# Optimization experiments

Hardware: AMD Instinct MI355X
Metric: run time of the kernel (lower is better)

Reference implementation:

```python
import jax, jax.numpy as jnp
import numpy as np

B, T, C, H, DI = 4, 1024, 1024, 16, 128
TAU = 1.0
LAMBDA_CONF = 0.1
SYS2_THR = 1.0


def _ln(x, w, b):
    mu = x.mean(-1, keepdims=True)
    var = x.var(-1, keepdims=True)
    return (x - mu) * jax.lax.rsqrt(var + 1e-5) * w + b


def setup_inputs() -> dict:
    key = jax.random.key(0)
    ks = jax.random.split(key, 16)
    s = lambda i, shape: jax.random.normal(ks[i], shape, jnp.float32) * 0.02
    return {
        "h": jax.random.normal(ks[0], (B, T, C), jnp.float32),
        "ln_w": jnp.ones((C,), jnp.float32), "ln_b": jnp.zeros((C,), jnp.float32),
        "w_q": s(1, (C, C)), "w_k": s(2, (C, C)), "w_v": s(3, (C, C)),
        "w_o": s(4, (C, C)), "b_o": jnp.zeros((C,), jnp.float32),
        "U": s(5, (C, DI)), "V": s(6, (DI, C)),
        "gamma_w": s(7, (C, 1)), "gamma_b": jnp.zeros((1,), jnp.float32),
        "mass_w": s(8, (C, 1)), "mass_b": jnp.zeros((1,), jnp.float32),
        "eps_w": s(9, (C, 1)), "eps_b": jnp.zeros((1,), jnp.float32),
        "lg_w1": s(10, (C, 4 * C)), "lg_b1": jnp.zeros((4 * C,), jnp.float32),
        "lg_w2": s(11, (4 * C, C)), "lg_b2": jnp.zeros((C,), jnp.float32),
        "mlp_w1": s(12, (C, 4 * C)), "mlp_b1": jnp.zeros((4 * C,), jnp.float32),
        "mlp_w2": s(13, (4 * C, C)), "mlp_b2": jnp.zeros((C,), jnp.float32),
    }


def reference(h, ln_w, ln_b, w_q, w_k, w_v, w_o, b_o, U, V,
              gamma_w, gamma_b, mass_w, mass_b, eps_w, eps_b,
              lg_w1, lg_b1, lg_w2, lg_b2, mlp_w1, mlp_b1, mlp_w2, mlp_b2):
    hd = C // H
    h_norm = _ln(h, ln_w, ln_b)

    # ---- HamiltonianAttention (conservative force field) ----
    q = (h_norm @ w_q).reshape(B, T, H, hd).transpose(0, 2, 1, 3)  # [B,H,T,hd]
    k = (h_norm @ w_k).reshape(B, T, H, hd).transpose(0, 2, 1, 3)
    v = (h_norm @ w_v).reshape(B, T, H, hd).transpose(0, 2, 1, 3)
    scores = jnp.einsum('bhqd,bhkd->bhqk', q, k) / (hd ** 0.5) / TAU
    attn = jax.nn.softmax(scores, axis=-1)
    force = jnp.einsum('bhqk,bhkd->bhqd', attn, v).transpose(0, 2, 1, 3).reshape(B, T, C)
    f_attn = force @ w_o + b_o

    # ---- total force, low-rank projection ----
    f_total = f_attn - LAMBDA_CONF * h_norm
    f_proj = f_total @ U                               # [B,T,DI]

    # ---- FSI (force stability index) ----
    h_mag = jnp.linalg.norm(h_norm, axis=-1)           # [B,T]
    f_mag = jnp.linalg.norm(f_proj, axis=-1)
    fsi = h_mag / (2.0 * f_mag + 1e-6)

    # ---- CognitiveGearbox: per-token mass / timestep ----
    mass = 1.0 + jax.nn.softplus(h @ mass_w + mass_b)  # [B,T,1], mass >= 1
    eps = jax.nn.sigmoid(h @ eps_w + eps_b)            # [B,T,1], eps in (0,1)
    gamma = jax.nn.sigmoid(h_norm @ gamma_w + gamma_b) # [B,T,1] damping gate

    # ---- fused AGI momentum recurrence: m_t = gamma_t*m_{t-1} + (eps_t/mass_t)*f_t ----
    def step(m, inps):
        f_t, g_t, e_t, ms_t = inps                     # [B,DI],[B,1],[B,1],[B,1]
        m = g_t * m + (e_t / ms_t) * f_t
        return m, m

    xs = (f_proj.transpose(1, 0, 2), gamma.transpose(1, 0, 2),
          eps.transpose(1, 0, 2), mass.transpose(1, 0, 2))
    m0 = jnp.zeros((B, DI), h.dtype)
    _, m_seq = jax.lax.scan(step, m0, xs)              # [T,B,DI]
    m_new = m_seq.transpose(1, 0, 2)                   # [B,T,DI]

    # ---- position update + system-2 correction + MLP ----
    velocity = m_new @ V                               # [B,T,C]
    h_new = h + eps * velocity
    hn2 = _ln(h_new, ln_w, ln_b)
    sys2 = jax.nn.gelu(hn2 @ lg_w1 + lg_b1, approximate=False) @ lg_w2 + lg_b2
    gate = jax.nn.sigmoid(mass - SYS2_THR)
    h_final = h_new + gate * sys2
    hn3 = _ln(h_final, ln_w, ln_b)
    h_final = h_final + (jax.nn.gelu(hn3 @ mlp_w1 + mlp_b1, approximate=False) @ mlp_w2 + mlp_b2)
    return (h_final, m_new, fsi)
```

## Files before the change

kernel.cpp:

```cpp
#include <hip/hip_runtime.h>
#include <hip/hip_bf16.h>
#include <math.h>

typedef __attribute__((ext_vector_type(8))) short bf16x8;
typedef __attribute__((ext_vector_type(4))) float f32x4;

#define DEVI __device__ __forceinline__

constexpr int B_ = 4, T_ = 1024, C_ = 1024, H_ = 16, HD_ = 64, DI_ = 128;
constexpr int NTOK = B_ * T_;
constexpr int C4 = 4 * C_;
constexpr int C3 = 3 * C_;
constexpr float LAMBDA_CONF = 0.1f;

DEVI short f2bf(float f) {
  unsigned u = __builtin_bit_cast(unsigned, f);
  u += 0x7fffu + ((u >> 16) & 1u);
  return (short)(u >> 16);
}
DEVI unsigned pk2(float a, float b) {
  return (unsigned)(unsigned short)f2bf(a) | ((unsigned)(unsigned short)f2bf(b) << 16);
}
DEVI float sigm(float x) { return 1.f / (1.f + __expf(-x)); }
DEVI float geluf(float x) { return 0.5f * x * (1.f + erff(x * 0.70710678118654752440f)); }

DEVI void gload16(const void* g, void* l) {
  __builtin_amdgcn_global_load_lds((const __attribute__((address_space(1))) unsigned*)g,
                                   (__attribute__((address_space(3))) unsigned*)l, 16, 0, 0);
}

template <int EPI>
DEVI void epi_store(void* Outp, const float* bias, const float* resid, const float* tokv,
                    int row, int col, int N, float v) {
  size_t idx = (size_t)row * N + col;
  if (EPI == 0) {
    ((float*)Outp)[idx] = v;
  } else if (EPI == 1) {
    ((short*)Outp)[idx] = f2bf(v);
  } else if (EPI == 2) {
    ((short*)Outp)[idx] = f2bf(v + bias[col] - LAMBDA_CONF * resid[idx]);
  } else if (EPI == 3) {
    ((float*)Outp)[idx] = resid[idx] + tokv[row] * v;
  } else if (EPI == 4) {
    float x = v + bias[col];
    ((short*)Outp)[idx] = f2bf(geluf(x));
  } else if (EPI == 5) {
    float x = v + bias[col];
    float g = sigm(tokv[row] - 1.f);
    ((float*)Outp)[idx] = resid[idx] + g * x;
  } else if (EPI == 6) {
    ((float*)Outp)[idx] = resid[idx] + v + bias[col];
  }
}

__global__ __launch_bounds__(256) void transpose_cvt(const float* __restrict__ W,
                                                     short* __restrict__ Wt, int K, int N) {
  __shared__ float s[32][33];
  int n0 = blockIdx.x * 32, k0 = blockIdx.y * 32;
  int tx = threadIdx.x & 31, ty = threadIdx.x >> 5;
#pragma unroll
  for (int i = 0; i < 4; i++)
    s[ty + i * 8][tx] = W[(size_t)(k0 + ty + i * 8) * N + n0 + tx];
  __syncthreads();
#pragma unroll
  for (int i = 0; i < 4; i++)
    Wt[(size_t)(n0 + ty + i * 8) * K + k0 + tx] = f2bf(s[tx][ty + i * 8]);
}

__global__ __launch_bounds__(256) void transpose_v(const short* __restrict__ QKV,
                                                   short* __restrict__ VT) {
  __shared__ short s[32][33];
  int bh = blockIdx.z;
  int b = bh >> 4, h = bh & 15;
  int t0 = blockIdx.x * 32, d0 = blockIdx.y * 32;
  int tx = threadIdx.x & 31, ty = threadIdx.x >> 5;
#pragma unroll
  for (int i = 0; i < 4; i++)
    s[ty + i * 8][tx] =
        QKV[(size_t)(b * T_ + t0 + ty + i * 8) * C3 + 2 * C_ + h * 64 + d0 + tx];
  __syncthreads();
#pragma unroll
  for (int i = 0; i < 4; i++)
    VT[((size_t)bh * 64 + d0 + ty + i * 8) * T_ + t0 + tx] = s[tx][ty + i * 8];
}

DEVI float blk_red(float v, volatile float* sm) {
  int lane = threadIdx.x & 63, wv = threadIdx.x >> 6;
#pragma unroll
  for (int o = 32; o; o >>= 1) v += __shfl_down(v, o);
  __syncthreads();
  if (lane == 0) sm[wv] = v;
  __syncthreads();
  return sm[0] + sm[1] + sm[2] + sm[3];
}

template <int FULL, int WF32>
__global__ __launch_bounds__(256) void ln_kernel(
    const float* __restrict__ X, const float* __restrict__ lnw, const float* __restrict__ lnb,
    float* __restrict__ Out, short* __restrict__ OutBf,
    const float* __restrict__ gw, const float* __restrict__ gb,
    const float* __restrict__ mw, const float* __restrict__ mb,
    const float* __restrict__ ew, const float* __restrict__ eb,
    float* __restrict__ gammaA, float* __restrict__ epsA, float* __restrict__ massA,
    float* __restrict__ coefA, float* __restrict__ hmagA) {
  __shared__ float sm[4];
  int tok = blockIdx.x;
  const float* x = X + (size_t)tok * C_;
  int t4 = threadIdx.x * 4;
  float4 xv = *(const float4*)&x[t4];
  float s = xv.x + xv.y + xv.z + xv.w;
  float ss = xv.x * xv.x + xv.y * xv.y + xv.z * xv.z + xv.w * xv.w;
  s = blk_red(s, sm);
  ss = blk_red(ss, sm);
  float mu = s * (1.f / C_);
  float var = ss * (1.f / C_) - mu * mu;
  float rs = rsqrtf(var + 1e-5f);
  float4 wv = *(const float4*)&lnw[t4];
  float4 bv = *(const float4*)&lnb[t4];
  float4 hn;
  hn.x = (xv.x - mu) * rs * wv.x + bv.x;
  hn.y = (xv.y - mu) * rs * wv.y + bv.y;
  hn.z = (xv.z - mu) * rs * wv.z + bv.z;
  hn.w = (xv.w - mu) * rs * wv.w + bv.w;
  if (WF32) *(float4*)&Out[(size_t)tok * C_ + t4] = hn;
  short4 ob;
  ob.x = f2bf(hn.x); ob.y = f2bf(hn.y); ob.z = f2bf(hn.z); ob.w = f2bf(hn.w);
  *(short4*)&OutBf[(size_t)tok * C_ + t4] = ob;
  if (FULL) {
    float4 gwv = *(const float4*)&gw[t4];
    float4 mwv = *(const float4*)&mw[t4];
    float4 ewv = *(const float4*)&ew[t4];
    float gd = hn.x * gwv.x + hn.y * gwv.y + hn.z * gwv.z + hn.w * gwv.w;
    float md = xv.x * mwv.x + xv.y * mwv.y + xv.z * mwv.z + xv.w * mwv.w;
    float ed = xv.x * ewv.x + xv.y * ewv.y + xv.z * ewv.z + xv.w * ewv.w;
    float h2 = hn.x * hn.x + hn.y * hn.y + hn.z * hn.z + hn.w * hn.w;
    gd = blk_red(gd, sm);
    md = blk_red(md, sm);
    ed = blk_red(ed, sm);
    h2 = blk_red(h2, sm);
    if (threadIdx.x == 0) {
      float g = sigm(gd + gb[0]);
      float xm = md + mb[0];
      float sp = (xm > 20.f) ? xm : log1pf(expf(xm));
      float msv = 1.f + sp;
      float epv = sigm(ed + eb[0]);
      gammaA[tok] = g;
      massA[tok] = msv;
      epsA[tok] = epv;
      coefA[tok] = epv / msv;
      hmagA[tok] = sqrtf(h2);
    }
  }
}

template <int EPI, int NB>
__global__ __launch_bounds__(256, 3) void gemmS(
    const short* __restrict__ A, const short* __restrict__ Bt, void* __restrict__ Outp,
    const float* __restrict__ bias, const float* __restrict__ resid,
    const float* __restrict__ tokv, int M, int N, int K) {
  constexpr int NT = NB / 64;
  constexpr int NFR = NB / 32;
  __shared__ short As[128][32];
  __shared__ short Bs[NB][32];
  int tid = threadIdx.x, lane = tid & 63, w = tid >> 6;
  int wr = w >> 1, wc = w & 1;
  int fr = lane & 15, fg = lane >> 4;
  int xm = (fr >> 1) & 3;
  int nM = M >> 7;
  int cpx = gridDim.x >> 3;
  int bid = (blockIdx.x & 7) * cpx + (blockIdx.x >> 3);
  int bm = (bid % nM) << 7;
  int bn = (bid / nM) * NB;
  f32x4 acc[4][NFR] = {};

  int jsw = (lane & 3) ^ ((lane >> 3) & 3);
  const short* gA = A + (size_t)(bm + w * 32 + (lane >> 2)) * K + (jsw << 3);
  const short* gB;
  if constexpr (NB == 128)
    gB = Bt + (size_t)(bn + w * 32 + (lane >> 2)) * K + (jsw << 3);
  else
    gB = Bt + (size_t)(bn + w * 16 + (lane >> 2)) * K + (jsw << 3);

  for (int kt = 0; kt < K; kt += 32) {
    gload16(gA + kt, &As[w * 32][0]);
    gload16(gA + (size_t)16 * K + kt, &As[w * 32 + 16][0]);
    if constexpr (NB == 128) {
      gload16(gB + kt, &Bs[w * 32][0]);
      gload16(gB + (size_t)16 * K + kt, &Bs[w * 32 + 16][0]);
    } else {
      gload16(gB + kt, &Bs[w * 16][0]);
    }
    __syncthreads();
    bf16x8 af[4], bv[NFR];
#pragma unroll
    for (int i = 0; i < 4; i++)
      af[i] = *(const bf16x8*)&As[wr * 64 + i * 16 + fr][(fg ^ xm) << 3];
#pragma unroll
    for (int j = 0; j < NFR; j++)
      bv[j] = *(const bf16x8*)&Bs[wc * (NB / 2) + j * 16 + fr][(fg ^ xm) << 3];
#pragma unroll
    for (int mi = 0; mi < 4; mi++)
#pragma unroll
      for (int ni = 0; ni < NFR; ni++)
        acc[mi][ni] = __builtin_amdgcn_mfma_f32_16x16x32_bf16(af[mi], bv[ni], acc[mi][ni], 0, 0, 0);
    __syncthreads();
  }

#pragma unroll
  for (int mi = 0; mi < 4; mi++) {
    int row0 = bm + wr * 64 + mi * 16 + fg * 4;
#pragma unroll
    for (int ni = 0; ni < NFR; ni++) {
      int col = bn + wc * (NB / 2) + ni * 16 + fr;
#pragma unroll
      for (int r = 0; r < 4; r++)
        epi_store<EPI>(Outp, bias, resid, tokv, row0 + r, col, N, acc[mi][ni][r]);
    }
  }
}

template <int EPI, int MT, int NT>
__global__ __launch_bounds__(512) void gemmP(
    const short* __restrict__ A, const short* __restrict__ Bt, void* __restrict__ Outp,
    const float* __restrict__ bias, const float* __restrict__ resid,
    const float* __restrict__ tokv, int M, int N, int K) {
  constexpr int BM = 4 * MT * 16;
  constexpr int BN = 2 * NT * 16;
  constexpr int CA = BM / 64;
  constexpr int CB = BN / 64;
  constexpr int LPT = CA + CB;
  __shared__ short As[3][BM][64];
  __shared__ short Bs[3][BN][64];
  int tid = threadIdx.x, lane = tid & 63, w = tid >> 6;
  int wr = w >> 1, wc = w & 1;
  int fr = lane & 15, fg = lane >> 4;
  int nMt = M / BM;
  int cpx = gridDim.x >> 3;
  int gbid = (blockIdx.x & 7) * cpx + (blockIdx.x >> 3);
  int chunk = gbid >> 5;
  int wi = gbid & 31;
  int nCM = nMt >> 2;
  int bm = ((chunk % nCM) * 4 + (wi & 3)) * BM;
  int bn = ((chunk / nCM) * 8 + (wi >> 2)) * BN;
  f32x4 acc[MT][NT] = {};

  int jsw = (lane & 7) ^ ((lane >> 3) & 7);
  const short* gA = A + (size_t)(bm + w * 8 + (lane >> 3)) * K + (jsw << 3);
  const short* gB = Bt + (size_t)(bn + w * 8 + (lane >> 3)) * K + (jsw << 3);

  auto stage = [&](int buf, int kt) {
#pragma unroll
    for (int c = 0; c < CA; c++)
      gload16(gA + (size_t)(c * 64) * K + kt, &As[buf][c * 64 + w * 8][0]);
#pragma unroll
    for (int c = 0; c < CB; c++)
      gload16(gB + (size_t)(c * 64) * K + kt, &Bs[buf][c * 64 + w * 8][0]);
  };

  int nt = K >> 6;
  stage(0, 0);
  if (nt > 1) stage(1, 64);
  for (int t = 0; t < nt; t++) {
    if (t + 1 < nt) {
      if constexpr (LPT == 6) asm volatile("s_waitcnt vmcnt(6)" ::: "memory");
      else asm volatile("s_waitcnt vmcnt(4)" ::: "memory");
    } else {
      asm volatile("s_waitcnt vmcnt(0)" ::: "memory");
    }
    __builtin_amdgcn_s_barrier();
    __builtin_amdgcn_sched_barrier(0);
    int nb = t + 2;
    if (nb < nt) stage(nb % 3, nb << 6);
    int cb = t % 3;
    short(*Ac)[64] = As[cb];
    short(*Bc)[64] = Bs[cb];
    bf16x8 af[MT], bv[NT / 2];
#pragma unroll
    for (int kh = 0; kh < 2; kh++) {
#pragma unroll
      for (int i = 0; i < MT; i++) {
        int row = wr * (MT * 16) + i * 16 + fr;
        af[i] = *(const bf16x8*)&Ac[row][((((kh << 2) | fg)) ^ (fr & 7)) << 3];
      }
#pragma unroll
      for (int nh = 0; nh < 2; nh++) {
#pragma unroll
        for (int j = 0; j < NT / 2; j++) {
          int row = wc * (NT * 16) + nh * (NT / 2) * 16 + j * 16 + fr;
          bv[j] = *(const bf16x8*)&Bc[row][((((kh << 2) | fg)) ^ (fr & 7)) << 3];
        }
#pragma unroll
        for (int i = 0; i < MT; i++)
#pragma unroll
          for (int j = 0; j < NT / 2; j++)
            acc[i][nh * (NT / 2) + j] = __builtin_amdgcn_mfma_f32_16x16x32_bf16(
                af[i], bv[j], acc[i][nh * (NT / 2) + j], 0, 0, 0);
      }
    }
  }

#pragma unroll
  for (int mi = 0; mi < MT; mi++) {
    int row0 = bm + wr * (MT * 16) + mi * 16 + fg * 4;
#pragma unroll
    for (int ni = 0; ni < NT; ni++) {
      int col = bn + wc * (NT * 16) + ni * 16 + fr;
#pragma unroll
      for (int r = 0; r < 4; r++)
        epi_store<EPI>(Outp, bias, resid, tokv, row0 + r, col, N, acc[mi][ni][r]);
    }
  }
}

template <int EPI>
__global__ __launch_bounds__(256) void gemm128(
    const short* __restrict__ A, const short* __restrict__ Bt, void* __restrict__ Outp,
    const float* __restrict__ bias, const float* __restrict__ resid,
    const float* __restrict__ tokv, int M, int N, int K) {
  __shared__ short As[3][128][32];
  __shared__ short Bs[3][128][32];
  int tid = threadIdx.x, lane = tid & 63, w = tid >> 6;
  int wr = w >> 1, wc = w & 1;
  int fr = lane & 15, fg = lane >> 4;
  int xm = (fr >> 1) & 3;
  int nM = M >> 7;
  int cpx = gridDim.x >> 3;
  int bid = (blockIdx.x & 7) * cpx + (blockIdx.x >> 3);
  int bm = (bid % nM) << 7;
  int bn = (bid / nM) << 7;
  f32x4 acc[4][4] = {};

  int jsw = (lane & 3) ^ ((lane >> 3) & 3);
  const short* gA = A + (size_t)(bm + w * 32 + (lane >> 2)) * K + (jsw << 3);
  const short* gB = Bt + (size_t)(bn + w * 32 + (lane >> 2)) * K + (jsw << 3);

  auto stage = [&](int buf, int kt) {
#pragma unroll
    for (int g = 0; g < 2; g++) {
      gload16(gA + (size_t)(g * 16) * K + kt, &As[buf][w * 32 + g * 16][0]);
      gload16(gB + (size_t)(g * 16) * K + kt, &Bs[buf][w * 32 + g * 16][0]);
    }
  };

  int nt = K >> 5;
  stage(0, 0);
  if (nt > 1) stage(1, 32);
  for (int t = 0; t < nt; t++) {
    if (t + 1 < nt) asm volatile("s_waitcnt vmcnt(4)" ::: "memory");
    else asm volatile("s_waitcnt vmcnt(0)" ::: "memory");
    __builtin_amdgcn_s_barrier();
    __builtin_amdgcn_sched_barrier(0);
    int nb = t + 2;
    if (nb < nt) stage(nb % 3, nb << 5);
    int cb = t % 3;
    bf16x8 af[4], bfv[4];
#pragma unroll
    for (int i = 0; i < 4; i++)
      af[i] = *(const bf16x8*)&As[cb][wr * 64 + i * 16 + fr][(fg ^ xm) << 3];
#pragma unroll
    for (int i = 0; i < 4; i++)
      bfv[i] = *(const bf16x8*)&Bs[cb][wc * 64 + i * 16 + fr][(fg ^ xm) << 3];
#pragma unroll
    for (int mi = 0; mi < 4; mi++)
#pragma unroll
      for (int ni = 0; ni < 4; ni++)
        acc[mi][ni] = __builtin_amdgcn_mfma_f32_16x16x32_bf16(af[mi], bfv[ni], acc[mi][ni], 0, 0, 0);
  }

#pragma unroll
  for (int mi = 0; mi < 4; mi++) {
    int row0 = bm + wr * 64 + mi * 16 + fg * 4;
#pragma unroll
    for (int ni = 0; ni < 4; ni++) {
      int col = bn + wc * 64 + ni * 16 + fr;
#pragma unroll
      for (int r = 0; r < 4; r++)
        epi_store<EPI>(Outp, bias, resid, tokv, row0 + r, col, N, acc[mi][ni][r]);
    }
  }
}

__global__ __launch_bounds__(256) void attn_kernel(const short* __restrict__ QKV,
                                                   const short* __restrict__ VT,
                                                   short* __restrict__ Fout) {
  __shared__ short Ks[2][64][64];
  __shared__ short Vts[2][64][64];
  __shared__ short Ps[4][16][72];
  int bh = blockIdx.y;
  int b = bh >> 4, h = bh & 15;
  int qt0 = blockIdx.x * 64;
  int tid = threadIdx.x, lane = tid & 63, w = tid >> 6;
  int fr = lane & 15, fg = lane >> 4;

  size_t base = ((size_t)b * T_) * C3 + h * 64;
  const short* Qp = QKV + base;
  const short* Kp = QKV + base + C_;
  const short* Vtp = VT + (size_t)bh * 64 * T_;
  int qrow = qt0 + w * 16 + fr;
  bf16x8 qf0 = *(const bf16x8*)&Qp[(size_t)qrow * C3 + fg * 8];
  bf16x8 qf1 = *(const bf16x8*)&Qp[(size_t)qrow * C3 + 32 + fg * 8];

  f32x4 oacc[4] = {};
  float m_run = -1e30f, l_run = 0.f;

  int jsw = (lane & 7) ^ ((lane >> 3) & 7);
  int sr8 = w * 8;
  int rsub = lane >> 3;

  auto stage = [&](int buf, int kt) {
#pragma unroll
    for (int c = 0; c < 2; c++) {
      int row = c * 32 + sr8 + rsub;
      gload16(Kp + (size_t)(kt + row) * C3 + jsw * 8, &Ks[buf][c * 32 + sr8][0]);
      gload16(Vtp + (size_t)row * T_ + kt + jsw * 8, &Vts[buf][c * 32 + sr8][0]);
    }
  };

  stage(0, 0);
  for (int t = 0; t < T_ / 64; t++) {
    if (t + 1 < T_ / 64) {
      stage((t + 1) & 1, (t + 1) * 64);
      asm volatile("s_waitcnt vmcnt(4)" ::: "memory");
    } else {
      asm volatile("s_waitcnt vmcnt(0)" ::: "memory");
    }
    __builtin_amdgcn_s_barrier();
    __builtin_amdgcn_sched_barrier(0);
    int cb = t & 1;

    f32x4 sacc[4];
#pragma unroll
    for (int kb = 0; kb < 4; kb++) {
      bf16x8 k0 = *(const bf16x8*)&Ks[cb][kb * 16 + fr][(fg ^ (fr & 7)) << 3];
      bf16x8 k1 = *(const bf16x8*)&Ks[cb][kb * 16 + fr][((4 | fg) ^ (fr & 7)) << 3];
      f32x4 z = {};
      z = __builtin_amdgcn_mfma_f32_16x16x32_bf16(k0, qf0, z, 0, 0, 0);
      z = __builtin_amdgcn_mfma_f32_16x16x32_bf16(k1, qf1, z, 0, 0, 0);
      sacc[kb] = z;
    }
    float mt = -1e30f;
#pragma unroll
    for (int kb = 0; kb < 4; kb++)
#pragma unroll
      for (int r = 0; r < 4; r++) {
        sacc[kb][r] *= 0.125f;
        mt = fmaxf(mt, sacc[kb][r]);
      }
    mt = fmaxf(mt, __shfl_xor(mt, 16));
    mt = fmaxf(mt, __shfl_xor(mt, 32));
    float m_new = fmaxf(m_run, mt);
    float alpha = __expf(m_run - m_new);
    float psum = 0.f;
    float pv[16];
#pragma unroll
    for (int kb = 0; kb < 4; kb++)
#pragma unroll
      for (int r = 0; r < 4; r++) {
        float p = __expf(sacc[kb][r] - m_new);
        pv[kb * 4 + r] = p;
        psum += p;
      }
    psum += __shfl_xor(psum, 16);
    psum += __shfl_xor(psum, 32);
    l_run = l_run * alpha + psum;
    m_run = m_new;

#pragma unroll
    for (int kb = 0; kb < 4; kb++) {
      uint2 pp;
      pp.x = pk2(pv[kb * 4 + 0], pv[kb * 4 + 1]);
      pp.y = pk2(pv[kb * 4 + 2], pv[kb * 4 + 3]);
      *(uint2*)&Ps[w][fr][kb * 16 + fg * 4] = pp;
    }
    float ar[4];
#pragma unroll
    for (int r = 0; r < 4; r++) ar[r] = __shfl(alpha, fg * 4 + r);
#pragma unroll
    for (int ni = 0; ni < 4; ni++)
#pragma unroll
      for (int r = 0; r < 4; r++) oacc[ni][r] *= ar[r];

    asm volatile("s_waitcnt lgkmcnt(0)" ::: "memory");
    __builtin_amdgcn_sched_barrier(0);
    bf16x8 pa0 = *(const bf16x8*)&Ps[w][fr][fg * 8];
    bf16x8 pa1 = *(const bf16x8*)&Ps[w][fr][32 + fg * 8];
#pragma unroll
    for (int ni = 0; ni < 4; ni++) {
      bf16x8 v0 = *(const bf16x8*)&Vts[cb][ni * 16 + fr][(fg ^ (fr & 7)) << 3];
      bf16x8 v1 = *(const bf16x8*)&Vts[cb][ni * 16 + fr][((4 | fg) ^ (fr & 7)) << 3];
      oacc[ni] = __builtin_amdgcn_mfma_f32_16x16x32_bf16(pa0, v0, oacc[ni], 0, 0, 0);
      oacc[ni] = __builtin_amdgcn_mfma_f32_16x16x32_bf16(pa1, v1, oacc[ni], 0, 0, 0);
    }
    __builtin_amdgcn_s_barrier();
  }

  float lr4[4];
#pragma unroll
  for (int r = 0; r < 4; r++) lr4[r] = __shfl(l_run, fg * 4 + r);
#pragma unroll
  for (int ni = 0; ni < 4; ni++)
#pragma unroll
    for (int r = 0; r < 4; r++) {
      int tok = b * T_ + qt0 + w * 16 + fg * 4 + r;
      Fout[(size_t)tok * C_ + h * 64 + ni * 16 + fr] = f2bf(oacc[ni][r] / lr4[r]);
    }
}

__global__ __launch_bounds__(128) void scan_kernel(const float* __restrict__ f_proj,
                                                   const float* __restrict__ gam,
                                                   const float* __restrict__ coef,
                                                   float* __restrict__ m_out,
                                                   short* __restrict__ m_bf) {
  int b = blockIdx.x;
  int d = threadIdx.x;
  const float* fp = f_proj + (size_t)b * T_ * DI_ + d;
  const float* g = gam + (size_t)b * T_;
  const float* c = coef + (size_t)b * T_;
  float* mo = m_out + (size_t)b * T_ * DI_ + d;
  short* mb = m_bf + (size_t)b * T_ * DI_ + d;
  float m = 0.f;
  for (int t = 0; t < T_; t += 8) {
    float fv[8], gv[8], cv[8];
#pragma unroll
    for (int i = 0; i < 8; i++) {
      fv[i] = fp[(size_t)(t + i) * DI_];
      gv[i] = g[t + i];
      cv[i] = c[t + i];
    }
#pragma unroll
    for (int i = 0; i < 8; i++) {
      m = gv[i] * m + cv[i] * fv[i];
      mo[(size_t)(t + i) * DI_] = m;
      mb[(size_t)(t + i) * DI_] = f2bf(m);
    }
  }
}

__global__ __launch_bounds__(256) void fsi_kernel(const float* __restrict__ f_proj,
                                                  const float* __restrict__ hmag,
                                                  float* __restrict__ fsi_out) {
  int tok = blockIdx.x * 4 + (threadIdx.x >> 6);
  int l = threadIdx.x & 63;
  float2 v = *(const float2*)&f_proj[(size_t)tok * DI_ + l * 2];
  float s = v.x * v.x + v.y * v.y;
#pragma unroll
  for (int o = 32; o; o >>= 1) s += __shfl_down(s, o);
  if (l == 0) fsi_out[tok] = hmag[tok] / (2.f * sqrtf(s) + 1e-6f);
}

extern "C" void kernel_launch(void* const* d_in, const int* in_sizes, int n_in,
                              void* d_out, int out_size, void* d_ws, size_t ws_size,
                              hipStream_t stream) {
  (void)in_sizes; (void)n_in; (void)out_size; (void)ws_size;
  const float* h = (const float*)d_in[0];
  const float* ln_w = (const float*)d_in[1];
  const float* ln_b = (const float*)d_in[2];
  const float* w_q = (const float*)d_in[3];
  const float* w_k = (const float*)d_in[4];
  const float* w_v = (const float*)d_in[5];
  const float* w_o = (const float*)d_in[6];
  const float* b_o = (const float*)d_in[7];
  const float* U = (const float*)d_in[8];
  const float* V = (const float*)d_in[9];
  const float* gamma_w = (const float*)d_in[10];
  const float* gamma_b = (const float*)d_in[11];
  const float* mass_w = (const float*)d_in[12];
  const float* mass_b = (const float*)d_in[13];
  const float* eps_w = (const float*)d_in[14];
  const float* eps_b = (const float*)d_in[15];
  const float* lg_w1 = (const float*)d_in[16];
  const float* lg_b1 = (const float*)d_in[17];
  const float* lg_w2 = (const float*)d_in[18];
  const float* lg_b2 = (const float*)d_in[19];
  const float* mlp_w1 = (const float*)d_in[20];
  const float* mlp_b1 = (const float*)d_in[21];
  const float* mlp_w2 = (const float*)d_in[22];
  const float* mlp_b2 = (const float*)d_in[23];

  float* out_h = (float*)d_out;
  float* out_m = out_h + (size_t)NTOK * C_;
  float* out_fsi = out_m + (size_t)NTOK * DI_;

  char* wsb = (char*)d_ws;
  size_t off = 0;
  auto al = [&](size_t bytes) {
    void* p = wsb + off;
    off += (bytes + 255) & ~(size_t)255;
    return p;
  };
  short* wqkvt = (short*)al((size_t)C3 * C_ * 2);
  short* wot = (short*)al((size_t)C_ * C_ * 2);
  short* ut = (short*)al((size_t)DI_ * C_ * 2);
  short* vt = (short*)al((size_t)C_ * DI_ * 2);
  short* lg1t = (short*)al((size_t)C4 * C_ * 2);
  short* lg2t = (short*)al((size_t)C_ * C4 * 2);
  short* mlp1t = (short*)al((size_t)C4 * C_ * 2);
  short* mlp2t = (short*)al((size_t)C_ * C4 * 2);
  float* h_norm = (float*)al((size_t)NTOK * C_ * 4);
  short* hn_bf = (short*)al((size_t)NTOK * C_ * 2);
  short* qkv_bf = (short*)al((size_t)NTOK * C3 * 2);
  short* tmp_bf = (short*)al((size_t)NTOK * C_ * 2);
  float* f_proj = (float*)al((size_t)NTOK * DI_ * 4);
  short* act = (short*)al((size_t)NTOK * C4 * 2);
  float* h_pre = (float*)al((size_t)NTOK * C_ * 4);
  short* vtrans = (short*)al((size_t)B_ * H_ * 64 * T_ * 2);
  float* gammaA = (float*)al((size_t)NTOK * 4);
  float* epsA = (float*)al((size_t)NTOK * 4);
  float* massA = (float*)al((size_t)NTOK * 4);
  float* coefA = (float*)al((size_t)NTOK * 4);
  float* hmagA = (float*)al((size_t)NTOK * 4);
  short* ftot_bf = hn_bf;
  short* m_bf = act;
  float* h_new = (float*)qkv_bf;

  dim3 blk(256);
  dim3 blk512(512);
  transpose_cvt<<<dim3(C_ / 32, C_ / 32), blk, 0, stream>>>(w_q, wqkvt, C_, C_);
  transpose_cvt<<<dim3(C_ / 32, C_ / 32), blk, 0, stream>>>(w_k, wqkvt + (size_t)C_ * C_, C_, C_);
  transpose_cvt<<<dim3(C_ / 32, C_ / 32), blk, 0, stream>>>(w_v, wqkvt + (size_t)2 * C_ * C_, C_, C_);
  transpose_cvt<<<dim3(C_ / 32, C_ / 32), blk, 0, stream>>>(w_o, wot, C_, C_);
  transpose_cvt<<<dim3(DI_ / 32, C_ / 32), blk, 0, stream>>>(U, ut, C_, DI_);
  transpose_cvt<<<dim3(C_ / 32, DI_ / 32), blk, 0, stream>>>(V, vt, DI_, C_);
  transpose_cvt<<<dim3(C4 / 32, C_ / 32), blk, 0, stream>>>(lg_w1, lg1t, C_, C4);
  transpose_cvt<<<dim3(C_ / 32, C4 / 32), blk, 0, stream>>>(lg_w2, lg2t, C4, C_);
  transpose_cvt<<<dim3(C4 / 32, C_ / 32), blk, 0, stream>>>(mlp_w1, mlp1t, C_, C4);
  transpose_cvt<<<dim3(C_ / 32, C4 / 32), blk, 0, stream>>>(mlp_w2, mlp2t, C4, C_);

  ln_kernel<1, 1><<<NTOK, blk, 0, stream>>>(h, ln_w, ln_b, h_norm, hn_bf, gamma_w, gamma_b,
                                            mass_w, mass_b, eps_w, eps_b, gammaA, epsA, massA,
                                            coefA, hmagA);
  gemmS<1, 128><<<(NTOK / 128) * (C3 / 128), blk, 0, stream>>>(hn_bf, wqkvt, qkv_bf, nullptr,
                                                               nullptr, nullptr, NTOK, C3, C_);
  transpose_v<<<dim3(T_ / 32, 2, B_ * H_), blk, 0, stream>>>(qkv_bf, vtrans);
  attn_kernel<<<dim3(T_ / 64, B_ * H_), blk, 0, stream>>>(qkv_bf, vtrans, tmp_bf);
  gemmP<2, 2, 4><<<(NTOK / 128) * (C_ / 128), blk512, 0, stream>>>(tmp_bf, wot, ftot_bf, b_o,
                                                                   h_norm, nullptr, NTOK, C_, C_);
  gemm128<0><<<(NTOK / 128) * (DI_ / 128), blk, 0, stream>>>(ftot_bf, ut, f_proj, nullptr,
                                                             nullptr, nullptr, NTOK, DI_, C_);
  fsi_kernel<<<NTOK / 4, blk, 0, stream>>>(f_proj, hmagA, out_fsi);
  scan_kernel<<<B_, dim3(DI_), 0, stream>>>(f_proj, gammaA, coefA, out_m, m_bf);
  gemmP<3, 2, 4><<<(NTOK / 128) * (C_ / 128), blk512, 0, stream>>>(m_bf, vt, h_new, nullptr, h,
                                                                   epsA, NTOK, C_, DI_);
  ln_kernel<0, 0><<<NTOK, blk, 0, stream>>>(h_new, ln_w, ln_b, nullptr, tmp_bf, nullptr, nullptr,
                                            nullptr, nullptr, nullptr, nullptr, nullptr, nullptr,
                                            nullptr, nullptr, nullptr);
  gemmS<4, 128><<<(NTOK / 128) * (C4 / 128), blk, 0, stream>>>(tmp_bf, lg1t, act, lg_b1,
                                                               nullptr, nullptr, NTOK, C4, C_);
  gemmS<5, 64><<<(NTOK / 128) * (C_ / 64), blk, 0, stream>>>(act, lg2t, h_pre, lg_b2,
                                                             h_new, massA, NTOK, C_, C4);
  ln_kernel<0, 0><<<NTOK, blk, 0, stream>>>(h_pre, ln_w, ln_b, nullptr, tmp_bf, nullptr, nullptr,
                                            nullptr, nullptr, nullptr, nullptr, nullptr, nullptr,
                                            nullptr, nullptr, nullptr);
  gemmS<4, 128><<<(NTOK / 128) * (C4 / 128), blk, 0, stream>>>(tmp_bf, mlp1t, act, mlp_b1,
                                                               nullptr, nullptr, NTOK, C4, C_);
  gemmS<6, 64><<<(NTOK / 128) * (C_ / 64), blk, 0, stream>>>(act, mlp2t, out_h, mlp_b2,
                                                             h_pre, nullptr, NTOK, C_, C4);
}
```

Baseline: 503.2 us.

## Triple-buffer gemmS loads with async prefetch and add trailing barriers to GEMM loops

```diff
diff --git a/kernel.cpp b/kernel.cpp
--- a/kernel.cpp
+++ b/kernel.cpp
@@ -158,10 +158,10 @@
     const short* __restrict__ A, const short* __restrict__ Bt, void* __restrict__ Outp,
     const float* __restrict__ bias, const float* __restrict__ resid,
     const float* __restrict__ tokv, int M, int N, int K) {
-  constexpr int NT = NB / 64;
   constexpr int NFR = NB / 32;
-  __shared__ short As[128][32];
-  __shared__ short Bs[NB][32];
+  constexpr int LPT = 2 + (NB == 128 ? 2 : 1);
+  __shared__ short As[3][128][32];
+  __shared__ short Bs[3][NB][32];
   int tid = threadIdx.x, lane = tid & 63, w = tid >> 6;
   int wr = w >> 1, wc = w & 1;
   int fr = lane & 15, fg = lane >> 4;
@@ -181,29 +181,46 @@
   else
     gB = Bt + (size_t)(bn + w * 16 + (lane >> 2)) * K + (jsw << 3);
 
-  for (int kt = 0; kt < K; kt += 32) {
-    gload16(gA + kt, &As[w * 32][0]);
-    gload16(gA + (size_t)16 * K + kt, &As[w * 32 + 16][0]);
+  auto stage = [&](int buf, int kt) {
+    gload16(gA + kt, &As[buf][w * 32][0]);
+    gload16(gA + (size_t)16 * K + kt, &As[buf][w * 32 + 16][0]);
     if constexpr (NB == 128) {
-      gload16(gB + kt, &Bs[w * 32][0]);
-      gload16(gB + (size_t)16 * K + kt, &Bs[w * 32 + 16][0]);
+      gload16(gB + kt, &Bs[buf][w * 32][0]);
+      gload16(gB + (size_t)16 * K + kt, &Bs[buf][w * 32 + 16][0]);
     } else {
-      gload16(gB + kt, &Bs[w * 16][0]);
-    }
-    __syncthreads();
+      gload16(gB + kt, &Bs[buf][w * 16][0]);
+    }
+  };
+
+  int nt = K >> 5;
+  stage(0, 0);
+  if (nt > 1) stage(1, 32);
+  for (int t = 0; t < nt; t++) {
+    if (t + 1 < nt) {
+      if constexpr (LPT == 4) asm volatile("s_waitcnt vmcnt(4)" ::: "memory");
+      else asm volatile("s_waitcnt vmcnt(3)" ::: "memory");
+    } else {
+      asm volatile("s_waitcnt vmcnt(0)" ::: "memory");
+    }
+    __builtin_amdgcn_s_barrier();
+    __builtin_amdgcn_sched_barrier(0);
+    int nb = t + 2;
+    if (nb < nt) stage(nb % 3, nb << 5);
+    int cb = t % 3;
     bf16x8 af[4], bv[NFR];
 #pragma unroll
     for (int i = 0; i < 4; i++)
-      af[i] = *(const bf16x8*)&As[wr * 64 + i * 16 + fr][(fg ^ xm) << 3];
+      af[i] = *(const bf16x8*)&As[cb][wr * 64 + i * 16 + fr][(fg ^ xm) << 3];
 #pragma unroll
     for (int j = 0; j < NFR; j++)
-      bv[j] = *(const bf16x8*)&Bs[wc * (NB / 2) + j * 16 + fr][(fg ^ xm) << 3];
+      bv[j] = *(const bf16x8*)&Bs[cb][wc * (NB / 2) + j * 16 + fr][(fg ^ xm) << 3];
 #pragma unroll
     for (int mi = 0; mi < 4; mi++)
 #pragma unroll
       for (int ni = 0; ni < NFR; ni++)
         acc[mi][ni] = __builtin_amdgcn_mfma_f32_16x16x32_bf16(af[mi], bv[ni], acc[mi][ni], 0, 0, 0);
-    __syncthreads();
+    __builtin_amdgcn_sched_barrier(0);
+    __builtin_amdgcn_s_barrier();
   }
 
 #pragma unroll
@@ -297,6 +314,8 @@
                 af[i], bv[j], acc[i][nh * (NT / 2) + j], 0, 0, 0);
       }
     }
+    __builtin_amdgcn_sched_barrier(0);
+    __builtin_amdgcn_s_barrier();
   }
 
 #pragma unroll
@@ -365,6 +384,8 @@
 #pragma unroll
       for (int ni = 0; ni < 4; ni++)
         acc[mi][ni] = __builtin_amdgcn_mfma_f32_16x16x32_bf16(af[mi], bfv[ni], acc[mi][ni], 0, 0, 0);
+    __builtin_amdgcn_sched_barrier(0);
+    __builtin_amdgcn_s_barrier();
   }
 
 #pragma unroll
@@ -491,6 +512,7 @@
       oacc[ni] = __builtin_amdgcn_mfma_f32_16x16x32_bf16(pa0, v0, oacc[ni], 0, 0, 0);
       oacc[ni] = __builtin_amdgcn_mfma_f32_16x16x32_bf16(pa1, v1, oacc[ni], 0, 0, 0);
     }
+    __builtin_amdgcn_sched_barrier(0);
     __builtin_amdgcn_s_barrier();
   }
 
```

After: 552.9 us. 9.9% more time.
